# Performance work log

Measured on AMD Instinct MI355X. Metric: run time of the kernel, lower is better.

## Reference

```python
import jax, jax.numpy as jnp
import numpy as np
import math

B, L, D_MODEL, H = 2, 2048, 2048, 16
HD = D_MODEL // H  # 128


def _rope(x):
    # x: (B,H,L,HD) interleaved-pair RoPE (GPT-NeoX / RoFormer style with ::2 strides)
    hd = x.shape[-1]
    inv_freq = 1.0 / (10000.0 ** (jnp.arange(0, hd, 2, dtype=jnp.float32) / hd))  # (HD/2,)
    t = jnp.arange(x.shape[2], dtype=jnp.float32)
    freqs = t[:, None] * inv_freq[None, :]            # (L, HD/2)
    cos = jnp.cos(freqs)[None, None]                  # (1,1,L,HD/2)
    sin = jnp.sin(freqs)[None, None]
    x1 = x[..., ::2]
    x2 = x[..., 1::2]
    even = x1 * cos - x2 * sin
    odd = x1 * sin + x2 * cos
    # interleave even/odd back: (...,HD/2,2) -> (...,HD)
    return jnp.stack([even, odd], axis=-1).reshape(x.shape)


def setup_inputs() -> dict:
    key = jax.random.key(0)
    k1, k2, k3, k4, k5, k6 = jax.random.split(key, 6)
    x_q = jax.random.normal(k1, (B, L, D_MODEL), dtype=jnp.float32)
    x_kv = jax.random.normal(k2, (B, L, D_MODEL), dtype=jnp.float32)
    # causal additive mask: 0 keep, -1e9 masked, broadcastable to (B,H,L,S)
    causal = jnp.tril(jnp.ones((L, L), dtype=bool))
    attn_mask = jnp.where(causal, 0.0, -1e9).astype(jnp.float32)[None, None]
    s = 0.02
    w_q = jax.random.normal(k3, (D_MODEL, D_MODEL), dtype=jnp.float32) * s
    w_k = jax.random.normal(k4, (D_MODEL, D_MODEL), dtype=jnp.float32) * s
    w_v = jax.random.normal(k5, (D_MODEL, D_MODEL), dtype=jnp.float32) * s
    w_o = jax.random.normal(k6, (D_MODEL, D_MODEL), dtype=jnp.float32) * s
    return {"x_q": x_q, "x_kv": x_kv, "attn_mask": attn_mask,
            "w_q": w_q, "w_k": w_k, "w_v": w_v, "w_o": w_o}


def _shape(x):
    b, l, _ = x.shape
    return x.reshape(b, l, H, HD).transpose(0, 2, 1, 3)  # (B,H,L,HD)


def reference(x_q, x_kv, attn_mask, w_q, w_k, w_v, w_o):
    # torch Linear (no bias): y = x @ W.T
    q = _shape(x_q @ w_q.T)
    k = _shape(x_kv @ w_k.T)
    v = _shape(x_kv @ w_v.T)
    q = _rope(q)
    k = _rope(k)
    scale = 1.0 / math.sqrt(HD)
    scores = jnp.einsum('bhld,bhsd->bhls', q, k) * scale + attn_mask
    attn = jax.nn.softmax(scores, axis=-1)            # (B,H,L,S)
    out = jnp.einsum('bhls,bhsd->bhld', attn, v)
    out = out.transpose(0, 2, 1, 3).reshape(x_q.shape[0], x_q.shape[1], H * HD)
    out = out @ w_o.T
    return (out, attn)
```

## Files before the change

kernel.cpp:

```cpp
#include <hip/hip_runtime.h>
#include <hip/hip_bf16.h>
#include <math.h>

#define B_ 2
#define L_ 2048
#define D_ 2048
#define H_ 16
#define HD_ 128
#define E_ (B_*L_*D_)
#define W_ (D_*D_)

typedef __bf16 bf16;
typedef __bf16 bf16x8 __attribute__((ext_vector_type(8)));
typedef __bf16 bf16x4 __attribute__((ext_vector_type(4)));
typedef float  f32x4  __attribute__((ext_vector_type(4)));

#define GLL16(gp_, lp_) __builtin_amdgcn_global_load_lds( \
    (const __attribute__((address_space(1))) void*)(gp_), \
    (__attribute__((address_space(3))) void*)(lp_), 16, 0, 0)

#define BARRIER() do { asm volatile("" ::: "memory"); \
    __builtin_amdgcn_s_barrier(); \
    asm volatile("" ::: "memory"); } while (0)

__global__ void cvt_f32_bf16(const float* __restrict__ src, bf16* __restrict__ dst, int n) {
  int i = (blockIdx.x * blockDim.x + threadIdx.x) * 4;
  if (i + 3 < n) {
    f32x4 v = *reinterpret_cast<const f32x4*>(src + i);
    bf16x4 o;
    o[0] = (bf16)v[0]; o[1] = (bf16)v[1]; o[2] = (bf16)v[2]; o[3] = (bf16)v[3];
    *reinterpret_cast<bf16x4*>(dst + i) = o;
  }
}

__global__ void rope_table(float* __restrict__ ct, float* __restrict__ st) {
  int t = blockIdx.x;
  int i = threadIdx.x;
  float inv = powf(10000.0f, -2.0f * (float)i / 128.0f);
  float f = (float)t * inv;
  ct[t * 64 + i] = cosf(f);
  st[t * 64 + i] = sinf(f);
}

__global__ void rope_inplace(bf16* __restrict__ Q, bf16* __restrict__ Kt,
                             const float* __restrict__ ct, const float* __restrict__ st) {
  size_t idx = (size_t)blockIdx.x * blockDim.x + threadIdx.x;
  const size_t per = E_ / 8;
  bf16* P = (idx < per) ? Q : Kt;
  size_t li = ((idx < per) ? idx : idx - per) * 8;
  int l   = (int)((li / D_) % L_);
  int col = (int)(li % D_);
  int i0  = (col & 127) >> 1;
  bf16x8 v = *reinterpret_cast<const bf16x8*>(P + li);
  f32x4 c4 = *reinterpret_cast<const f32x4*>(ct + l * 64 + i0);
  f32x4 s4 = *reinterpret_cast<const f32x4*>(st + l * 64 + i0);
  bf16x8 o;
#pragma unroll
  for (int p = 0; p < 4; ++p) {
    float x1 = (float)v[2*p], x2 = (float)v[2*p+1];
    o[2*p]   = (bf16)(x1 * c4[p] - x2 * s4[p]);
    o[2*p+1] = (bf16)(x1 * s4[p] + x2 * c4[p]);
  }
  *reinterpret_cast<bf16x8*>(P + li) = o;
}

__global__ void transpose_v(const bf16* __restrict__ Vraw, bf16* __restrict__ Vt) {
  __shared__ bf16 tile[32][33];
  int bh = blockIdx.z; int b = bh >> 4, h = bh & 15;
  int l0 = blockIdx.x * 32, d0 = blockIdx.y * 32;
  int tx = threadIdx.x, ty = threadIdx.y;
#pragma unroll
  for (int j = 0; j < 4; ++j) {
    int r = ty + j * 8;
    tile[r][tx] = Vraw[((size_t)b * L_ + l0 + r) * D_ + h * HD_ + d0 + tx];
  }
  __syncthreads();
#pragma unroll
  for (int j = 0; j < 4; ++j) {
    int r = ty + j * 8;
    Vt[((size_t)bh * HD_ + d0 + r) * L_ + l0 + tx] = tile[tx][r];
  }
}

__global__ void zero_upper(float* __restrict__ attn) {
  int l = blockIdx.x, bh = blockIdx.y;
  int z0 = ((l >> 6) + 1) << 6;
  float* row = attn + ((size_t)bh * L_ + l) * L_;
  for (int c = z0 + threadIdx.x * 4; c < L_; c += 256 * 4) {
    *reinterpret_cast<f32x4*>(row + c) = (f32x4){0.f, 0.f, 0.f, 0.f};
  }
}

template<int OUT_BF16>
__global__ __launch_bounds__(256, 4) void gemm_bt(const bf16* __restrict__ A,
                                                  const bf16* __restrict__ Bw,
                                                  void* __restrict__ Cout,
                                                  int M, int N, int K) {
  __shared__ bf16 As[128 * 64];
  __shared__ bf16 Bs[128 * 64];
  const int tid = threadIdx.x;
  const int lane = tid & 63;
  const int w = tid >> 6;
  const int l15 = lane & 15, lg = lane >> 4;
  const int m0 = blockIdx.y * 128, n0 = blockIdx.x * 128;
  const int wm = (w >> 1) * 64, wn = (w & 1) * 64;

  int rowS[4], schS[4];
#pragma unroll
  for (int s = 0; s < 4; ++s) {
    int cl = s * 256 + tid;
    rowS[s] = cl >> 3;
    schS[s] = ((cl & 7) ^ ((cl >> 3) & 7)) << 3;
  }

  f32x4 acc[4][4];
#pragma unroll
  for (int m = 0; m < 4; ++m)
#pragma unroll
    for (int n = 0; n < 4; ++n) acc[m][n] = (f32x4){0.f, 0.f, 0.f, 0.f};

  for (int kt = 0; kt < K; kt += 64) {
    __syncthreads();
#pragma unroll
    for (int s = 0; s < 4; ++s) {
      GLL16(A  + (size_t)(m0 + rowS[s]) * K + kt + schS[s], As + s * 2048 + w * 512);
      GLL16(Bw + (size_t)(n0 + rowS[s]) * K + kt + schS[s], Bs + s * 2048 + w * 512);
    }
    __syncthreads();
#pragma unroll
    for (int kk = 0; kk < 64; kk += 32) {
      bf16x8 af[4], bfr[4];
#pragma unroll
      for (int m = 0; m < 4; ++m)
        af[m] = *reinterpret_cast<const bf16x8*>(
            As + (wm + m * 16 + l15) * 64 + ((((kk >> 3) + lg) ^ (l15 & 7)) << 3));
#pragma unroll
      for (int n = 0; n < 4; ++n)
        bfr[n] = *reinterpret_cast<const bf16x8*>(
            Bs + (wn + n * 16 + l15) * 64 + ((((kk >> 3) + lg) ^ (l15 & 7)) << 3));
#pragma unroll
      for (int m = 0; m < 4; ++m)
#pragma unroll
        for (int n = 0; n < 4; ++n)
          acc[m][n] = __builtin_amdgcn_mfma_f32_16x16x32_bf16(af[m], bfr[n], acc[m][n], 0, 0, 0);
    }
  }
#pragma unroll
  for (int m = 0; m < 4; ++m) {
    int orow = m0 + wm + m * 16 + lg * 4;
#pragma unroll
    for (int n = 0; n < 4; ++n) {
      int col = n0 + wn + n * 16 + l15;
#pragma unroll
      for (int r = 0; r < 4; ++r) {
        if (OUT_BF16) ((bf16*)Cout)[(size_t)(orow + r) * N + col] = (bf16)acc[m][n][r];
        else          ((float*)Cout)[(size_t)(orow + r) * N + col] = acc[m][n][r];
      }
    }
  }
}

__global__ __launch_bounds__(512, 4) void attn_fused(const bf16* __restrict__ Qb,
                                                     const bf16* __restrict__ Kb,
                                                     const bf16* __restrict__ Vt,
                                                     float* __restrict__ attn,
                                                     bf16* __restrict__ Oh) {
  __shared__ bf16 Klds[2][64 * 128];
  __shared__ bf16 Vlds[128 * 64];
  __shared__ bf16 Plds[8][16][72];

  const int tid = threadIdx.x;
  const int w = tid >> 6, lane = tid & 63;
  const int l15 = lane & 15, lg = lane >> 4;
  const int bh = blockIdx.y, b = bh >> 4, h = bh & 15;
  const int x = blockIdx.x;
  const int qt = (w < 4) ? x : (31 - x);
  const int q0w = qt * 64 + (w & 3) * 16;
  const int ntW = qt + 1;
  const int ntB = 32 - x;
  const float sc2 = 0.08838834764831845f * 1.44269504088896f;

  const bf16* kb = Kb + ((size_t)b * L_) * D_ + h * HD_;
  const bf16* vb = Vt + (size_t)bh * HD_ * L_;

  bf16x8 qf[4];
  {
    const bf16* qrow = Qb + ((size_t)b * L_ + q0w + l15) * D_ + h * HD_;
#pragma unroll
    for (int c = 0; c < 4; ++c)
      qf[c] = *reinterpret_cast<const bf16x8*>(qrow + c * 32 + lg * 8);
  }

  const int t1 = 512 + tid;
  const int rK0 = tid >> 4, sK0 = ((tid & 15) ^ (rK0 & 7)) << 3;
  const int rK1 = t1 >> 4,  sK1 = ((t1 & 15) ^ (rK1 & 7)) << 3;
  const int rV0 = tid >> 3, sV0 = ((tid & 7) ^ (rV0 & 7)) << 3;
  const int rV1 = t1 >> 3,  sV1 = ((t1 & 7) ^ (rV1 & 7)) << 3;
  bf16* ldsK0 = &Klds[0][0] + w * 512;
  bf16* ldsK1 = &Klds[0][0] + 4096 + w * 512;
  bf16* ldsV0 = Vlds + w * 512;
  bf16* ldsV1 = Vlds + 4096 + w * 512;

  auto stageK = [&](int gp, int buf) {
    GLL16(kb + (size_t)(gp * 64 + rK0) * D_ + sK0, ldsK0 + buf * 8192);
    GLL16(kb + (size_t)(gp * 64 + rK1) * D_ + sK1, ldsK1 + buf * 8192);
  };
  auto stageV = [&](int gp) {
    GLL16(vb + (size_t)rV0 * L_ + gp * 64 + sV0, ldsV0);
    GLL16(vb + (size_t)rV1 * L_ + gp * 64 + sV1, ldsV1);
  };
  auto qkt = [&](const bf16* kl, f32x4* acc) {
#pragma unroll
    for (int c = 0; c < 4; ++c)
#pragma unroll
      for (int t = 0; t < 4; ++t) {
        bf16x8 kf = *reinterpret_cast<const bf16x8*>(
            kl + (t * 16 + l15) * 128 + ((((c << 2) + lg) ^ (l15 & 7)) << 3));
        acc[t] = __builtin_amdgcn_mfma_f32_16x16x32_bf16(qf[c], kf, acc[t], 0, 0, 0);
      }
  };

  float sum[4] = {0.f, 0.f, 0.f, 0.f};
  stageK(0, 0);
  for (int gp = 0; gp < ntB; ++gp) {
    BARRIER();
    if (gp + 1 < ntB) {
      stageK(gp + 1, (gp + 1) & 1);
      asm volatile("s_waitcnt vmcnt(2)" ::: "memory");
    } else {
      asm volatile("s_waitcnt vmcnt(0)" ::: "memory");
    }
    BARRIER();
    if (gp < ntW) {
      f32x4 acc[4] = {(f32x4){0,0,0,0},(f32x4){0,0,0,0},(f32x4){0,0,0,0},(f32x4){0,0,0,0}};
      qkt(&Klds[gp & 1][0], acc);
      if (gp < qt) {
#pragma unroll
        for (int t = 0; t < 4; ++t)
#pragma unroll
          for (int r = 0; r < 4; ++r)
            sum[r] += exp2f(acc[t][r] * sc2);
      } else {
#pragma unroll
        for (int t = 0; t < 4; ++t)
#pragma unroll
          for (int r = 0; r < 4; ++r) {
            int kc = gp * 64 + t * 16 + l15;
            int qr = q0w + lg * 4 + r;
            sum[r] += (kc <= qr) ? exp2f(acc[t][r] * sc2) : 0.f;
          }
      }
    }
  }
#pragma unroll
  for (int r = 0; r < 4; ++r) {
#pragma unroll
    for (int sh = 1; sh < 16; sh <<= 1)
      sum[r] += __shfl_xor(sum[r], sh, 64);
  }
  float rinv[4];
#pragma unroll
  for (int r = 0; r < 4; ++r) rinv[r] = 1.0f / sum[r];

  f32x4 oacc[8];
#pragma unroll
  for (int i = 0; i < 8; ++i) oacc[i] = (f32x4){0.f, 0.f, 0.f, 0.f};
  float* arow = attn + ((size_t)bh * L_ + q0w) * L_;

  BARRIER();
  stageK(0, 0);
  for (int gp = 0; gp < ntB; ++gp) {
    BARRIER();
    stageV(gp);
    if (gp + 1 < ntB) {
      stageK(gp + 1, (gp + 1) & 1);
      asm volatile("s_waitcnt vmcnt(4)" ::: "memory");
    } else {
      asm volatile("s_waitcnt vmcnt(2)" ::: "memory");
    }
    BARRIER();
    const bool act = gp < ntW;
    float pv[4][4];
    if (act) {
      f32x4 acc[4] = {(f32x4){0,0,0,0},(f32x4){0,0,0,0},(f32x4){0,0,0,0},(f32x4){0,0,0,0}};
      qkt(&Klds[gp & 1][0], acc);
      if (gp < qt) {
#pragma unroll
        for (int t = 0; t < 4; ++t)
#pragma unroll
          for (int r = 0; r < 4; ++r)
            pv[t][r] = exp2f(acc[t][r] * sc2) * rinv[r];
      } else {
#pragma unroll
        for (int t = 0; t < 4; ++t)
#pragma unroll
          for (int r = 0; r < 4; ++r) {
            int kc = gp * 64 + t * 16 + l15;
            int qr = q0w + lg * 4 + r;
            pv[t][r] = (kc <= qr) ? exp2f(acc[t][r] * sc2) * rinv[r] : 0.f;
          }
      }
#pragma unroll
      for (int t = 0; t < 4; ++t)
#pragma unroll
        for (int r = 0; r < 4; ++r)
          Plds[w][lg * 4 + r][t * 16 + l15] = (bf16)pv[t][r];
    }
    if (gp + 1 < ntB) asm volatile("s_waitcnt vmcnt(2)" ::: "memory");
    else              asm volatile("s_waitcnt vmcnt(0)" ::: "memory");
    if (act) {
#pragma unroll
      for (int t = 0; t < 4; ++t)
#pragma unroll
        for (int r = 0; r < 4; ++r)
          arow[(size_t)(lg * 4 + r) * L_ + gp * 64 + t * 16 + l15] = pv[t][r];
    }
    BARRIER();
    if (act) {
#pragma unroll
      for (int ck = 0; ck < 2; ++ck) {
        bf16x8 pa = *reinterpret_cast<const bf16x8*>(&Plds[w][l15][ck * 32 + lg * 8]);
#pragma unroll
        for (int t8 = 0; t8 < 8; ++t8) {
          bf16x8 vf = *reinterpret_cast<const bf16x8*>(
              Vlds + (t8 * 16 + l15) * 64 + ((((ck << 2) + lg) ^ (l15 & 7)) << 3));
          oacc[t8] = __builtin_amdgcn_mfma_f32_16x16x32_bf16(pa, vf, oacc[t8], 0, 0, 0);
        }
      }
    }
  }

  bf16* orow = Oh + ((size_t)b * L_ + q0w) * D_ + h * HD_;
#pragma unroll
  for (int t8 = 0; t8 < 8; ++t8)
#pragma unroll
    for (int r = 0; r < 4; ++r)
      orow[(size_t)(lg * 4 + r) * D_ + t8 * 16 + l15] = (bf16)oacc[t8][r];
}

extern "C" void kernel_launch(void* const* d_in, const int* in_sizes, int n_in,
                              void* d_out, int out_size, void* d_ws, size_t ws_size,
                              hipStream_t stream) {
  const float* x_q  = (const float*)d_in[0];
  const float* x_kv = (const float*)d_in[1];
  const float* w_q = (const float*)d_in[3];
  const float* w_k = (const float*)d_in[4];
  const float* w_v = (const float*)d_in[5];
  const float* w_o = (const float*)d_in[6];

  char* p = (char*)d_ws;
  auto alloc = [&](size_t bytes) { char* r = p; p += (bytes + 255) & ~(size_t)255; return r; };
  bf16* xq_b  = (bf16*)alloc((size_t)E_ * 2);
  bf16* xkv_b = (bf16*)alloc((size_t)E_ * 2);
  bf16* wq_b  = (bf16*)alloc((size_t)W_ * 2);
  bf16* wk_b  = (bf16*)alloc((size_t)W_ * 2);
  bf16* wv_b  = (bf16*)alloc((size_t)W_ * 2);
  bf16* wo_b  = (bf16*)alloc((size_t)W_ * 2);
  bf16* Qraw  = (bf16*)alloc((size_t)E_ * 2);
  bf16* Kraw  = (bf16*)alloc((size_t)E_ * 2);
  bf16* Vraw  = (bf16*)alloc((size_t)E_ * 2);
  bf16* Vt    = (bf16*)alloc((size_t)E_ * 2);
  bf16* Oh    = (bf16*)alloc((size_t)E_ * 2);
  float* ct   = (float*)alloc((size_t)L_ * 64 * 4);
  float* st2  = (float*)alloc((size_t)L_ * 64 * 4);

  float* out0     = (float*)d_out;
  float* attn_out = out0 + E_;

  cvt_f32_bf16<<<8192, 256, 0, stream>>>(x_q,  xq_b,  E_);
  cvt_f32_bf16<<<8192, 256, 0, stream>>>(x_kv, xkv_b, E_);
  cvt_f32_bf16<<<4096, 256, 0, stream>>>(w_q, wq_b, W_);
  cvt_f32_bf16<<<4096, 256, 0, stream>>>(w_k, wk_b, W_);
  cvt_f32_bf16<<<4096, 256, 0, stream>>>(w_v, wv_b, W_);
  cvt_f32_bf16<<<4096, 256, 0, stream>>>(w_o, wo_b, W_);
  rope_table<<<L_, 64, 0, stream>>>(ct, st2);

  gemm_bt<1><<<dim3(16, 32), 256, 0, stream>>>(xq_b,  wq_b, Qraw, B_*L_, D_, D_);
  gemm_bt<1><<<dim3(16, 32), 256, 0, stream>>>(xkv_b, wk_b, Kraw, B_*L_, D_, D_);
  gemm_bt<1><<<dim3(16, 32), 256, 0, stream>>>(xkv_b, wv_b, Vraw, B_*L_, D_, D_);

  rope_inplace<<<8192, 256, 0, stream>>>(Qraw, Kraw, ct, st2);
  transpose_v<<<dim3(64, 4, 32), dim3(32, 8), 0, stream>>>(Vraw, Vt);
  zero_upper<<<dim3(2048, 32), 256, 0, stream>>>(attn_out);
  attn_fused<<<dim3(16, 32), 512, 0, stream>>>(Qraw, Kraw, Vt, attn_out, Oh);
  gemm_bt<0><<<dim3(16, 32), 256, 0, stream>>>(Oh, wo_b, out0, B_*L_, D_, D_);
}
```

Before: 488.9 us.

## Fuse upper-triangle zeroing into attention kernel and batch conversion launches

Removes the separate zero_upper kernel and writes the masked-out zero probabilities from inside attn_fused: during the denominator pass for tiles past the diagonal, and in a tail loop for tiles beyond the block range. Hand-tuned vmcnt waits are adjusted to account for those extra stores. It also merges the six f32-to-bf16 conversion launches into two, and remaps block indices so the second batch's query tiles run in reverse order. The aim is to cut a full pass over the attention output and some launch overhead, at the cost of fragile manual waitcnt bookkeeping and extra stores in the attention kernel.

Result: faster. 477.5 us (-2.3%).

```diff
diff --git a/kernel.cpp b/kernel.cpp
--- a/kernel.cpp
+++ b/kernel.cpp
@@ -23,13 +23,37 @@
     __builtin_amdgcn_s_barrier(); \
     asm volatile("" ::: "memory"); } while (0)
 
-__global__ void cvt_f32_bf16(const float* __restrict__ src, bf16* __restrict__ dst, int n) {
+#define WAITN(N) asm volatile("s_waitcnt vmcnt(" #N ")" ::: "memory")
+
+__global__ void cvt2(const float* __restrict__ s0, const float* __restrict__ s1,
+                     bf16* __restrict__ d0, bf16* __restrict__ d1, int n) {
+  const float* s = blockIdx.y ? s1 : s0;
+  bf16* d = blockIdx.y ? d1 : d0;
   int i = (blockIdx.x * blockDim.x + threadIdx.x) * 4;
   if (i + 3 < n) {
-    f32x4 v = *reinterpret_cast<const f32x4*>(src + i);
+    f32x4 v = *reinterpret_cast<const f32x4*>(s + i);
     bf16x4 o;
     o[0] = (bf16)v[0]; o[1] = (bf16)v[1]; o[2] = (bf16)v[2]; o[3] = (bf16)v[3];
-    *reinterpret_cast<bf16x4*>(dst + i) = o;
+    *reinterpret_cast<bf16x4*>(d + i) = o;
+  }
+}
+__global__ void cvt4(const float* __restrict__ s0, const float* __restrict__ s1,
+                     const float* __restrict__ s2, const float* __restrict__ s3,
+                     bf16* __restrict__ d0, bf16* __restrict__ d1,
+                     bf16* __restrict__ d2, bf16* __restrict__ d3, int n) {
+  const float* s; bf16* d;
+  switch (blockIdx.y) {
+    case 0: s = s0; d = d0; break;
+    case 1: s = s1; d = d1; break;
+    case 2: s = s2; d = d2; break;
+    default: s = s3; d = d3; break;
+  }
+  int i = (blockIdx.x * blockDim.x + threadIdx.x) * 4;
+  if (i + 3 < n) {
+    f32x4 v = *reinterpret_cast<const f32x4*>(s + i);
+    bf16x4 o;
+    o[0] = (bf16)v[0]; o[1] = (bf16)v[1]; o[2] = (bf16)v[2]; o[3] = (bf16)v[3];
+    *reinterpret_cast<bf16x4*>(d + i) = o;
   }
 }
 
@@ -82,15 +106,6 @@
   }
 }
 
-__global__ void zero_upper(float* __restrict__ attn) {
-  int l = blockIdx.x, bh = blockIdx.y;
-  int z0 = ((l >> 6) + 1) << 6;
-  float* row = attn + ((size_t)bh * L_ + l) * L_;
-  for (int c = z0 + threadIdx.x * 4; c < L_; c += 256 * 4) {
-    *reinterpret_cast<f32x4*>(row + c) = (f32x4){0.f, 0.f, 0.f, 0.f};
-  }
-}
-
 template<int OUT_BF16>
 __global__ __launch_bounds__(256, 4) void gemm_bt(const bf16* __restrict__ A,
                                                   const bf16* __restrict__ Bw,
@@ -172,8 +187,13 @@
   const int tid = threadIdx.x;
   const int w = tid >> 6, lane = tid & 63;
   const int l15 = lane & 15, lg = lane >> 4;
-  const int bh = blockIdx.y, b = bh >> 4, h = bh & 15;
-  const int x = blockIdx.x;
+
+  int g = blockIdx.x + 16 * blockIdx.y;
+  int x, bh;
+  if (g < 256) { x = g & 15;        bh = g >> 4; }
+  else { int h2 = g - 256; x = 15 - (h2 & 15); bh = 16 + (h2 >> 4); }
+  const int b = bh >> 4, h = bh & 15;
+
   const int qt = (w < 4) ? x : (31 - x);
   const int q0w = qt * 64 + (w & 3) * 16;
   const int ntW = qt + 1;
@@ -182,6 +202,7 @@
 
   const bf16* kb = Kb + ((size_t)b * L_) * D_ + h * HD_;
   const bf16* vb = Vt + (size_t)bh * HD_ * L_;
+  float* arow = attn + ((size_t)bh * L_ + q0w) * L_;
 
   bf16x8 qf[4];
   {
@@ -224,12 +245,11 @@
   stageK(0, 0);
   for (int gp = 0; gp < ntB; ++gp) {
     BARRIER();
-    if (gp + 1 < ntB) {
-      stageK(gp + 1, (gp + 1) & 1);
-      asm volatile("s_waitcnt vmcnt(2)" ::: "memory");
-    } else {
-      asm volatile("s_waitcnt vmcnt(0)" ::: "memory");
-    }
+    const bool hn = (gp + 1 < ntB);
+    if (hn) stageK(gp + 1, (gp + 1) & 1);
+    const bool pz = (gp > 0) && ((gp - 1) >= ntW);
+    if (pz) { if (hn) WAITN(18); else WAITN(16); }
+    else    { if (hn) WAITN(2);  else WAITN(0);  }
     BARRIER();
     if (gp < ntW) {
       f32x4 acc[4] = {(f32x4){0,0,0,0},(f32x4){0,0,0,0},(f32x4){0,0,0,0},(f32x4){0,0,0,0}};
@@ -250,6 +270,12 @@
             sum[r] += (kc <= qr) ? exp2f(acc[t][r] * sc2) : 0.f;
           }
       }
+    } else {
+#pragma unroll
+      for (int t = 0; t < 4; ++t)
+#pragma unroll
+        for (int r = 0; r < 4; ++r)
+          arow[(size_t)(lg * 4 + r) * L_ + gp * 64 + t * 16 + l15] = 0.f;
     }
   }
 #pragma unroll
@@ -265,19 +291,17 @@
   f32x4 oacc[8];
 #pragma unroll
   for (int i = 0; i < 8; ++i) oacc[i] = (f32x4){0.f, 0.f, 0.f, 0.f};
-  float* arow = attn + ((size_t)bh * L_ + q0w) * L_;
 
   BARRIER();
   stageK(0, 0);
   for (int gp = 0; gp < ntB; ++gp) {
     BARRIER();
     stageV(gp);
-    if (gp + 1 < ntB) {
-      stageK(gp + 1, (gp + 1) & 1);
-      asm volatile("s_waitcnt vmcnt(4)" ::: "memory");
-    } else {
-      asm volatile("s_waitcnt vmcnt(2)" ::: "memory");
-    }
+    const bool hn = (gp + 1 < ntB);
+    if (hn) stageK(gp + 1, (gp + 1) & 1);
+    const bool ps = (gp > 0) && ((gp - 1) < ntW);
+    if (ps) { if (hn) WAITN(20); else WAITN(18); }
+    else    { if (hn) WAITN(4);  else WAITN(2);  }
     BARRIER();
     const bool act = gp < ntW;
     float pv[4][4];
@@ -306,8 +330,7 @@
         for (int r = 0; r < 4; ++r)
           Plds[w][lg * 4 + r][t * 16 + l15] = (bf16)pv[t][r];
     }
-    if (gp + 1 < ntB) asm volatile("s_waitcnt vmcnt(2)" ::: "memory");
-    else              asm volatile("s_waitcnt vmcnt(0)" ::: "memory");
+    if (hn) WAITN(2); else WAITN(0);
     if (act) {
 #pragma unroll
       for (int t = 0; t < 4; ++t)
@@ -317,6 +340,8 @@
     }
     BARRIER();
     if (act) {
+      asm volatile("s_waitcnt lgkmcnt(0)" ::: "memory");
+      __builtin_amdgcn_sched_barrier(0);
 #pragma unroll
       for (int ck = 0; ck < 2; ++ck) {
         bf16x8 pa = *reinterpret_cast<const bf16x8*>(&Plds[w][l15][ck * 32 + lg * 8]);
@@ -327,7 +352,15 @@
           oacc[t8] = __builtin_amdgcn_mfma_f32_16x16x32_bf16(pa, vf, oacc[t8], 0, 0, 0);
         }
       }
-    }
+      asm volatile("s_waitcnt lgkmcnt(0)" ::: "memory");
+    }
+  }
+
+  for (int gp2 = ntB; gp2 < 32; ++gp2) {
+#pragma unroll
+    for (int it = 0; it < 4; ++it)
+      *reinterpret_cast<f32x4*>(arow + (size_t)l15 * L_ + gp2 * 64 + lg * 4 + it * 16)
+          = (f32x4){0.f, 0.f, 0.f, 0.f};
   }
 
   bf16* orow = Oh + ((size_t)b * L_ + q0w) * D_ + h * HD_;
@@ -367,12 +400,8 @@
   float* out0     = (float*)d_out;
   float* attn_out = out0 + E_;
 
-  cvt_f32_bf16<<<8192, 256, 0, stream>>>(x_q,  xq_b,  E_);
-  cvt_f32_bf16<<<8192, 256, 0, stream>>>(x_kv, xkv_b, E_);
-  cvt_f32_bf16<<<4096, 256, 0, stream>>>(w_q, wq_b, W_);
-  cvt_f32_bf16<<<4096, 256, 0, stream>>>(w_k, wk_b, W_);
-  cvt_f32_bf16<<<4096, 256, 0, stream>>>(w_v, wv_b, W_);
-  cvt_f32_bf16<<<4096, 256, 0, stream>>>(w_o, wo_b, W_);
+  cvt2<<<dim3(8192, 2), 256, 0, stream>>>(x_q, x_kv, xq_b, xkv_b, E_);
+  cvt4<<<dim3(4096, 4), 256, 0, stream>>>(w_q, w_k, w_v, w_o, wq_b, wk_b, wv_b, wo_b, W_);
   rope_table<<<L_, 64, 0, stream>>>(ct, st2);
 
   gemm_bt<1><<<dim3(16, 32), 256, 0, stream>>>(xq_b,  wq_b, Qraw, B_*L_, D_, D_);
@@ -381,7 +410,6 @@
 
   rope_inplace<<<8192, 256, 0, stream>>>(Qraw, Kraw, ct, st2);
   transpose_v<<<dim3(64, 4, 32), dim3(32, 8), 0, stream>>>(Vraw, Vt);
-  zero_upper<<<dim3(2048, 32), 256, 0, stream>>>(attn_out);
   attn_fused<<<dim3(16, 32), 512, 0, stream>>>(Qraw, Kraw, Vt, attn_out, Oh);
   gemm_bt<0><<<dim3(16, 32), 256, 0, stream>>>(Oh, wo_b, out0, B_*L_, D_, D_);
 }
```
